# Performance work log

Hardware: AMD Instinct MI355X
Metric: run time of the kernel (lower is better)

The kernel has to match this reference:

```python
import jax, jax.numpy as jnp
import numpy as np

N = 100000   # nodes
E = 1600000  # edges
F = 128      # feature dim == Dense units
R = 50       # relations
BN_EPS = 1e-3  # keras BatchNormalization default epsilon


def setup_inputs() -> dict:
    key = jax.random.key(0)
    ks = jax.random.split(key, 8)
    x = jax.random.normal(ks[0], (N, F), dtype=jnp.float32)
    edge_rows = jax.random.randint(ks[1], (E,), 0, N, dtype=jnp.int32)
    edge_cols = jax.random.randint(ks[2], (E,), 0, N, dtype=jnp.int32)
    edge_vals = jax.random.uniform(ks[3], (E,), dtype=jnp.float32)
    rel_ids = jax.random.randint(ks[4], (E,), 0, R, dtype=jnp.int32)
    relation_coeffs = jax.random.uniform(ks[5], (R,), dtype=jnp.float32)
    coeff_kernel = jax.random.normal(ks[6], (N, 1), dtype=jnp.float32) * 0.05
    dense_kernel = jax.random.normal(ks[7], (F, F), dtype=jnp.float32) / np.sqrt(F).astype(np.float32)
    dense_bias = jnp.zeros((F,), dtype=jnp.float32)
    bn_gamma = jnp.ones((F,), dtype=jnp.float32)
    bn_beta = jnp.zeros((F,), dtype=jnp.float32)
    bn_mean = jnp.zeros((F,), dtype=jnp.float32)
    bn_var = jnp.ones((F,), dtype=jnp.float32)
    return {
        "x": x, "edge_rows": edge_rows, "edge_cols": edge_cols,
        "edge_vals": edge_vals, "rel_ids": rel_ids,
        "relation_coeffs": relation_coeffs, "coeff_kernel": coeff_kernel,
        "dense_kernel": dense_kernel, "dense_bias": dense_bias,
        "bn_gamma": bn_gamma, "bn_beta": bn_beta,
        "bn_mean": bn_mean, "bn_var": bn_var,
    }


def reference(x, edge_rows, edge_cols, edge_vals, rel_ids,
              relation_coeffs, coeff_kernel, dense_kernel, dense_bias,
              bn_gamma, bn_beta, bn_mean, bn_var):
    # BatchNorm (inference: moving statistics)
    h = (x - bn_mean) * jax.lax.rsqrt(bn_var + BN_EPS) * bn_gamma + bn_beta  # [N, F]
    # relation_coeff_adj2: edge weight = A.values * (rel_coeffs[rel] + 1)^-1
    w = edge_vals / (relation_coeffs[rel_ids] + 1.0)  # [E]
    # SpMM: out[i] = sum_{(i,j) in edges} w_e * h[j]
    msgs = w[:, None] * h[edge_cols]                   # [E, F]
    agg = jax.ops.segment_sum(msgs, edge_rows, num_segments=N)  # [N, F]
    # CoeffLayer(mul=True): inputs * (kernel + 1)
    pre = agg + h * (coeff_kernel + 1.0)               # [N, F]
    # Dense
    return pre @ dense_kernel + dense_bias             # [N, F]
```

## Files before the change

kernel.cpp:

```cpp
#include <hip/hip_runtime.h>
#include <stdint.h>

#define N_NODES 100000
#define N_EDGES 1600000
#define FDIM 128
#define NREL 50
#define BN_EPS 1e-3f
#define N_PAD 100096
#define NBUCK 782
#define EPB 8192
#define NBLK 196
#define HBLK 6250
#define LEDCAP 2816
#define SLACK 384
#define SCAP 3200
#define NSG 6250

typedef short short8_t __attribute__((ext_vector_type(8)));
typedef float f32x4_t __attribute__((ext_vector_type(4)));

__device__ __forceinline__ uint32_t f2bf(float f) {
    union { float f; uint32_t u; } v; v.f = f;
    uint32_t u = v.u;
    return (u + 0x7FFFu + ((u >> 16) & 1u)) >> 16;
}
__device__ __forceinline__ float bflo(uint32_t p) {
    union { uint32_t u; float f; } v; v.u = p << 16; return v.f;
}
__device__ __forceinline__ float bfhi(uint32_t p) {
    union { uint32_t u; float f; } v; v.u = p & 0xFFFF0000u; return v.f;
}

__global__ __launch_bounds__(512) void pre_kernel(
        const float* __restrict__ x, const int* __restrict__ rows,
        const int* __restrict__ cols, const float* __restrict__ vals,
        const int* __restrict__ rels, const float* __restrict__ relc,
        const float* __restrict__ gamma, const float* __restrict__ beta,
        const float* __restrict__ mean, const float* __restrict__ var,
        const float* __restrict__ W,
        uint2* __restrict__ h, uint16_t* __restrict__ WT,
        int* __restrict__ gcur, uint2* __restrict__ staging) {
    __shared__ int lh[NBUCK];
    __shared__ float lrel[NREL];
    int b = blockIdx.x, t = threadIdx.x;
    if (b < NBLK) {
        if (t < NREL) lrel[t] = 1.0f / (relc[t] + 1.0f);
        for (int i = t; i < NBUCK; i += 512) lh[i] = 0;
        __syncthreads();
        int e0 = b * EPB, e1 = min(e0 + EPB, N_EDGES);
        for (int e = e0 + t; e < e1; e += 512)
            atomicAdd(&lh[rows[e] >> 7], 1);
        __syncthreads();
        for (int i = t; i < NBUCK; i += 512) {
            int c = lh[i];
            int base = c ? atomicAdd(&gcur[i], c) : 0;
            lh[i] = i * SCAP + base;
        }
        __syncthreads();
        for (int e = e0 + t; e < e1; e += 512) {
            int r = rows[e];
            float w = vals[e] * lrel[rels[e]];
            int p = atomicAdd(&lh[r >> 7], 1);
            uint2 s;
            s.x = (uint32_t)cols[e] | ((uint32_t)(r & 127) << 20);
            s.y = __float_as_uint(w);
            staging[p] = s;
        }
    } else if (b == NBLK) {
        for (int idx = t; idx < FDIM * FDIM; idx += 512) {
            int f = idx >> 7, k = idx & 127;
            WT[idx] = (uint16_t)f2bf(W[k * FDIM + f]);
        }
    } else {
        int i4 = (b - NBLK - 1) * 512 + t;
        int cg = (i4 & 31) * 4;
        float4 xv = ((const float4*)x)[i4];
        float4 g4 = *(const float4*)(gamma + cg);
        float4 b4 = *(const float4*)(beta + cg);
        float4 m4 = *(const float4*)(mean + cg);
        float4 v4 = *(const float4*)(var + cg);
        float s0 = g4.x * rsqrtf(v4.x + BN_EPS);
        float s1 = g4.y * rsqrtf(v4.y + BN_EPS);
        float s2 = g4.z * rsqrtf(v4.z + BN_EPS);
        float s3 = g4.w * rsqrtf(v4.w + BN_EPS);
        uint2 o;
        o.x = f2bf((xv.x - m4.x) * s0 + b4.x) | (f2bf((xv.y - m4.y) * s1 + b4.y) << 16);
        o.y = f2bf((xv.z - m4.z) * s2 + b4.z) | (f2bf((xv.w - m4.w) * s3 + b4.w) << 16);
        h[i4] = o;
    }
}

__global__ __launch_bounds__(256) void bucket_kernel(
        const int* __restrict__ gcur, uint2* __restrict__ staging,
        uint2* __restrict__ rowrange) {
    __shared__ uint2 led[LEDCAP];
    __shared__ int lh[128];
    __shared__ int sm[128];
    __shared__ int lcur[128];
    int b = blockIdx.x, r0 = b << 7, t = threadIdx.x;
    int nrows = min(128, N_NODES - r0);
    int cnt = min(gcur[b], LEDCAP);
    uint2* sg = staging + (size_t)b * SCAP;
    if (t < 128) lh[t] = 0;
    __syncthreads();
    for (int e = t; e < cnt; e += 256) {
        uint2 s = sg[e];
        led[e] = s;
        atomicAdd(&lh[(s.x >> 20) & 127], 1);
    }
    __syncthreads();
    int v = (t < 128) ? lh[t] : 0;
    int pv = (v + 3) & ~3;
    if (t < 128) sm[t] = pv;
    __syncthreads();
    for (int off = 1; off < 128; off <<= 1) {
        int xv = 0;
        if (t < 128 && t >= off) xv = sm[t - off];
        __syncthreads();
        if (t < 128) sm[t] += xv;
        __syncthreads();
    }
    int sbase = b * SCAP;
    int start = 0;
    if (t < 128) {
        start = sbase + sm[t] - pv;
        lcur[t] = start;
        if (t < nrows) {
            uint2 rr; rr.x = (uint32_t)start; rr.y = (uint32_t)(start + pv);
            rowrange[r0 + t] = rr;
        }
    }
    __syncthreads();
    for (int e = t; e < cnt; e += 256) {
        uint2 s = led[e];
        int rl = (s.x >> 20) & 127;
        int p = atomicAdd(&lcur[rl], 1);
        uint2 o; o.x = s.x & 0xFFFFF; o.y = s.y;
        staging[p] = o;
    }
    if (t < 128) {
        uint2 z; z.x = 0; z.y = 0;
        for (int k = v; k < pv; ++k) staging[start + k] = z;
    }
}

__global__ __launch_bounds__(512, 8) void sg_kernel(
        const uint32_t* __restrict__ h, const uint2* __restrict__ rowrange,
        const uint2* __restrict__ scolw, const float* __restrict__ ck,
        const uint16_t* __restrict__ WT, const float* __restrict__ bias,
        float* __restrict__ out) {
    __shared__ uint32_t lp[16 * 64];
    int wv = threadIdx.x >> 6;
    int lane = threadIdx.x & 63;
    int row0 = blockIdx.x * 16;
    int rA = row0 + wv * 2, rB = rA + 1;

    uint2 ra = rowrange[rA];
    uint2 rb = rowrange[rB];
    int eA  = __builtin_amdgcn_readfirstlane((int)ra.x);
    int e1A = __builtin_amdgcn_readfirstlane((int)ra.y);
    int eB  = __builtin_amdgcn_readfirstlane((int)rb.x);
    int e1B = __builtin_amdgcn_readfirstlane((int)rb.y);
    uint32_t pA = h[(uint32_t)rA * 64u + lane];
    uint32_t pB = h[(uint32_t)rB * 64u + lane];
    float cA = ck[rA] + 1.0f, cB = ck[rB] + 1.0f;
    float axA = cA * bflo(pA), ayA = cA * bfhi(pA);
    float axB = cB * bflo(pB), ayB = cB * bfhi(pB);

    while (eA < e1A && eB < e1B) {
        const uint4* pa = (const uint4*)(scolw + eA);
        const uint4* pb = (const uint4*)(scolw + eB);
        uint4 a0 = pa[0], a1 = pa[1];
        uint4 b0 = pb[0], b1 = pb[1];
        uint32_t qa0 = h[a0.x * 64u + lane];
        uint32_t qa1 = h[a0.z * 64u + lane];
        uint32_t qa2 = h[a1.x * 64u + lane];
        uint32_t qa3 = h[a1.z * 64u + lane];
        uint32_t qb0 = h[b0.x * 64u + lane];
        uint32_t qb1 = h[b0.z * 64u + lane];
        uint32_t qb2 = h[b1.x * 64u + lane];
        uint32_t qb3 = h[b1.z * 64u + lane];
        float wa0 = __uint_as_float(a0.y), wa1 = __uint_as_float(a0.w);
        float wa2 = __uint_as_float(a1.y), wa3 = __uint_as_float(a1.w);
        float wb0 = __uint_as_float(b0.y), wb1 = __uint_as_float(b0.w);
        float wb2 = __uint_as_float(b1.y), wb3 = __uint_as_float(b1.w);
        axA += wa0 * bflo(qa0); ayA += wa0 * bfhi(qa0);
        axA += wa1 * bflo(qa1); ayA += wa1 * bfhi(qa1);
        axA += wa2 * bflo(qa2); ayA += wa2 * bfhi(qa2);
        axA += wa3 * bflo(qa3); ayA += wa3 * bfhi(qa3);
        axB += wb0 * bflo(qb0); ayB += wb0 * bfhi(qb0);
        axB += wb1 * bflo(qb1); ayB += wb1 * bfhi(qb1);
        axB += wb2 * bflo(qb2); ayB += wb2 * bfhi(qb2);
        axB += wb3 * bflo(qb3); ayB += wb3 * bfhi(qb3);
        eA += 4; eB += 4;
    }
    while (eA < e1A) {
        const uint4* pa = (const uint4*)(scolw + eA);
        uint4 a0 = pa[0], a1 = pa[1];
        uint32_t qa0 = h[a0.x * 64u + lane];
        uint32_t qa1 = h[a0.z * 64u + lane];
        uint32_t qa2 = h[a1.x * 64u + lane];
        uint32_t qa3 = h[a1.z * 64u + lane];
        float wa0 = __uint_as_float(a0.y), wa1 = __uint_as_float(a0.w);
        float wa2 = __uint_as_float(a1.y), wa3 = __uint_as_float(a1.w);
        axA += wa0 * bflo(qa0); ayA += wa0 * bfhi(qa0);
        axA += wa1 * bflo(qa1); ayA += wa1 * bfhi(qa1);
        axA += wa2 * bflo(qa2); ayA += wa2 * bfhi(qa2);
        axA += wa3 * bflo(qa3); ayA += wa3 * bfhi(qa3);
        eA += 4;
    }
    while (eB < e1B) {
        const uint4* pb = (const uint4*)(scolw + eB);
        uint4 b0 = pb[0], b1 = pb[1];
        uint32_t qb0 = h[b0.x * 64u + lane];
        uint32_t qb1 = h[b0.z * 64u + lane];
        uint32_t qb2 = h[b1.x * 64u + lane];
        uint32_t qb3 = h[b1.z * 64u + lane];
        float wb0 = __uint_as_float(b0.y), wb1 = __uint_as_float(b0.w);
        float wb2 = __uint_as_float(b1.y), wb3 = __uint_as_float(b1.w);
        axB += wb0 * bflo(qb0); ayB += wb0 * bfhi(qb0);
        axB += wb1 * bflo(qb1); ayB += wb1 * bfhi(qb1);
        axB += wb2 * bflo(qb2); ayB += wb2 * bfhi(qb2);
        axB += wb3 * bflo(qb3); ayB += wb3 * bfhi(qb3);
        eB += 4;
    }
    int rlA = wv * 2, rlB = rlA + 1;
    lp[rlA * 64 + (lane ^ ((rlA & 7) << 2))] = f2bf(axA) | (f2bf(ayA) << 16);
    lp[rlB * 64 + (lane ^ ((rlB & 7) << 2))] = f2bf(axB) | (f2bf(ayB) << 16);
    __syncthreads();

    int m = lane & 15, q = lane >> 4;
    short8_t a[4];
#pragma unroll
    for (int t = 0; t < 4; ++t) {
        int w0 = (q * 4 + t * 16) ^ ((m & 7) << 2);
        a[t] = *(const short8_t*)&lp[m * 64 + w0];
    }
    int col0 = wv * 16;
    const uint16_t* brow = WT + (size_t)(col0 + m) * FDIM + q * 8;
    f32x4_t acc = {0.f, 0.f, 0.f, 0.f};
#pragma unroll
    for (int t = 0; t < 4; ++t) {
        short8_t bb = *(const short8_t*)(brow + t * 32);
        acc = __builtin_amdgcn_mfma_f32_16x16x32_bf16(a[t], bb, acc, 0, 0, 0);
    }
    float bs = bias[col0 + m];
#pragma unroll
    for (int r = 0; r < 4; ++r)
        out[(size_t)(row0 + q * 4 + r) * FDIM + col0 + m] = acc[r] + bs;
}

extern "C" void kernel_launch(void* const* d_in, const int* in_sizes, int n_in,
                              void* d_out, int out_size, void* d_ws, size_t ws_size,
                              hipStream_t stream) {
    const float* x     = (const float*)d_in[0];
    const int*   erows = (const int*)d_in[1];
    const int*   ecols = (const int*)d_in[2];
    const float* evals = (const float*)d_in[3];
    const int*   erels = (const int*)d_in[4];
    const float* relc  = (const float*)d_in[5];
    const float* ck    = (const float*)d_in[6];
    const float* W     = (const float*)d_in[7];
    const float* bias  = (const float*)d_in[8];
    const float* gamma = (const float*)d_in[9];
    const float* beta  = (const float*)d_in[10];
    const float* mean  = (const float*)d_in[11];
    const float* var   = (const float*)d_in[12];
    float* out = (float*)d_out;

    char* wp = (char*)d_ws;
    auto alloc = [&](size_t bytes) {
        char* p = wp;
        wp += (bytes + 255) & ~(size_t)255;
        return (void*)p;
    };
    uint16_t* h      = (uint16_t*)alloc((size_t)N_PAD * FDIM * 2);
    uint2* staging   = (uint2*)alloc((size_t)NBUCK * SCAP * 8);
    uint2* rowrange  = (uint2*)alloc((size_t)N_PAD * 8);
    int* gcur        = (int*)alloc((size_t)NBUCK * 4);
    uint16_t* WT     = (uint16_t*)alloc(FDIM * FDIM * 2);
    if ((size_t)(wp - (char*)d_ws) > ws_size) return;

    hipMemsetAsync(gcur, 0, (size_t)NBUCK * 4, stream);
    pre_kernel<<<NBLK + 1 + HBLK, 512, 0, stream>>>(
        x, erows, ecols, evals, erels, relc, gamma, beta, mean, var, W,
        (uint2*)h, WT, gcur, staging);
    bucket_kernel<<<NBUCK, 256, 0, stream>>>(gcur, staging, rowrange);
    sg_kernel<<<NSG, 512, 0, stream>>>((const uint32_t*)h, rowrange, staging, ck,
                                       WT, bias, out);
}
```

Before: 259.9 us.

## Fuse per-bucket row sort into gather kernel using LDS-resident sorted edges

Removes the separate bucket_kernel. Buckets shrink to 64 rows, and each sg_kernel block now counting-sorts its bucket's edges into shared memory, then gathers and runs the MFMA dense projection for 64 rows. This drops one launch and the global write and re-read of the sorted staging buffer and row ranges. In exchange, occupancy drops because each block uses much more LDS and runs fewer, heavier blocks, and edges beyond SCAP per bucket are silently dropped.

```diff
diff --git a/kernel.cpp b/kernel.cpp
--- a/kernel.cpp
+++ b/kernel.cpp
@@ -7,14 +7,12 @@
 #define NREL 50
 #define BN_EPS 1e-3f
 #define N_PAD 100096
-#define NBUCK 782
+#define NBUCK 1563
 #define EPB 8192
 #define NBLK 196
 #define HBLK 6250
-#define LEDCAP 2816
-#define SLACK 384
-#define SCAP 3200
-#define NSG 6250
+#define SCAP 1536
+#define SORTN 1792
 
 typedef short short8_t __attribute__((ext_vector_type(8)));
 typedef float f32x4_t __attribute__((ext_vector_type(4)));
@@ -49,7 +47,7 @@
         __syncthreads();
         int e0 = b * EPB, e1 = min(e0 + EPB, N_EDGES);
         for (int e = e0 + t; e < e1; e += 512)
-            atomicAdd(&lh[rows[e] >> 7], 1);
+            atomicAdd(&lh[rows[e] >> 6], 1);
         __syncthreads();
         for (int i = t; i < NBUCK; i += 512) {
             int c = lh[i];
@@ -59,12 +57,15 @@
         __syncthreads();
         for (int e = e0 + t; e < e1; e += 512) {
             int r = rows[e];
+            int bk = r >> 6;
             float w = vals[e] * lrel[rels[e]];
-            int p = atomicAdd(&lh[r >> 7], 1);
-            uint2 s;
-            s.x = (uint32_t)cols[e] | ((uint32_t)(r & 127) << 20);
-            s.y = __float_as_uint(w);
-            staging[p] = s;
+            int p = atomicAdd(&lh[bk], 1);
+            if (p < (bk + 1) * SCAP) {
+                uint2 s;
+                s.x = (uint32_t)cols[e] | ((uint32_t)(r & 63) << 20);
+                s.y = __float_as_uint(w);
+                staging[p] = s;
+            }
         }
     } else if (b == NBLK) {
         for (int idx = t; idx < FDIM * FDIM; idx += 512) {
@@ -90,164 +91,167 @@
     }
 }
 
-__global__ __launch_bounds__(256) void bucket_kernel(
-        const int* __restrict__ gcur, uint2* __restrict__ staging,
-        uint2* __restrict__ rowrange) {
-    __shared__ uint2 led[LEDCAP];
-    __shared__ int lh[128];
-    __shared__ int sm[128];
-    __shared__ int lcur[128];
-    int b = blockIdx.x, r0 = b << 7, t = threadIdx.x;
-    int nrows = min(128, N_NODES - r0);
-    int cnt = min(gcur[b], LEDCAP);
-    uint2* sg = staging + (size_t)b * SCAP;
-    if (t < 128) lh[t] = 0;
-    __syncthreads();
-    for (int e = t; e < cnt; e += 256) {
-        uint2 s = sg[e];
-        led[e] = s;
-        atomicAdd(&lh[(s.x >> 20) & 127], 1);
-    }
-    __syncthreads();
-    int v = (t < 128) ? lh[t] : 0;
-    int pv = (v + 3) & ~3;
-    if (t < 128) sm[t] = pv;
-    __syncthreads();
-    for (int off = 1; off < 128; off <<= 1) {
-        int xv = 0;
-        if (t < 128 && t >= off) xv = sm[t - off];
-        __syncthreads();
-        if (t < 128) sm[t] += xv;
-        __syncthreads();
-    }
-    int sbase = b * SCAP;
-    int start = 0;
-    if (t < 128) {
-        start = sbase + sm[t] - pv;
-        lcur[t] = start;
-        if (t < nrows) {
-            uint2 rr; rr.x = (uint32_t)start; rr.y = (uint32_t)(start + pv);
-            rowrange[r0 + t] = rr;
-        }
-    }
-    __syncthreads();
-    for (int e = t; e < cnt; e += 256) {
-        uint2 s = led[e];
-        int rl = (s.x >> 20) & 127;
-        int p = atomicAdd(&lcur[rl], 1);
-        uint2 o; o.x = s.x & 0xFFFFF; o.y = s.y;
-        staging[p] = o;
-    }
-    if (t < 128) {
-        uint2 z; z.x = 0; z.y = 0;
-        for (int k = v; k < pv; ++k) staging[start + k] = z;
-    }
-}
-
 __global__ __launch_bounds__(512, 8) void sg_kernel(
-        const uint32_t* __restrict__ h, const uint2* __restrict__ rowrange,
-        const uint2* __restrict__ scolw, const float* __restrict__ ck,
+        const uint32_t* __restrict__ h, const int* __restrict__ gcur,
+        const uint2* __restrict__ staging, const float* __restrict__ ck,
         const uint16_t* __restrict__ WT, const float* __restrict__ bias,
         float* __restrict__ out) {
-    __shared__ uint32_t lp[16 * 64];
-    int wv = threadIdx.x >> 6;
-    int lane = threadIdx.x & 63;
-    int row0 = blockIdx.x * 16;
-    int rA = row0 + wv * 2, rB = rA + 1;
-
-    uint2 ra = rowrange[rA];
-    uint2 rb = rowrange[rB];
-    int eA  = __builtin_amdgcn_readfirstlane((int)ra.x);
-    int e1A = __builtin_amdgcn_readfirstlane((int)ra.y);
-    int eB  = __builtin_amdgcn_readfirstlane((int)rb.x);
-    int e1B = __builtin_amdgcn_readfirstlane((int)rb.y);
-    uint32_t pA = h[(uint32_t)rA * 64u + lane];
-    uint32_t pB = h[(uint32_t)rB * 64u + lane];
-    float cA = ck[rA] + 1.0f, cB = ck[rB] + 1.0f;
-    float axA = cA * bflo(pA), ayA = cA * bfhi(pA);
-    float axB = cB * bflo(pB), ayB = cB * bfhi(pB);
-
-    while (eA < e1A && eB < e1B) {
-        const uint4* pa = (const uint4*)(scolw + eA);
-        const uint4* pb = (const uint4*)(scolw + eB);
-        uint4 a0 = pa[0], a1 = pa[1];
-        uint4 b0 = pb[0], b1 = pb[1];
-        uint32_t qa0 = h[a0.x * 64u + lane];
-        uint32_t qa1 = h[a0.z * 64u + lane];
-        uint32_t qa2 = h[a1.x * 64u + lane];
-        uint32_t qa3 = h[a1.z * 64u + lane];
-        uint32_t qb0 = h[b0.x * 64u + lane];
-        uint32_t qb1 = h[b0.z * 64u + lane];
-        uint32_t qb2 = h[b1.x * 64u + lane];
-        uint32_t qb3 = h[b1.z * 64u + lane];
-        float wa0 = __uint_as_float(a0.y), wa1 = __uint_as_float(a0.w);
-        float wa2 = __uint_as_float(a1.y), wa3 = __uint_as_float(a1.w);
-        float wb0 = __uint_as_float(b0.y), wb1 = __uint_as_float(b0.w);
-        float wb2 = __uint_as_float(b1.y), wb3 = __uint_as_float(b1.w);
-        axA += wa0 * bflo(qa0); ayA += wa0 * bfhi(qa0);
-        axA += wa1 * bflo(qa1); ayA += wa1 * bfhi(qa1);
-        axA += wa2 * bflo(qa2); ayA += wa2 * bfhi(qa2);
-        axA += wa3 * bflo(qa3); ayA += wa3 * bfhi(qa3);
-        axB += wb0 * bflo(qb0); ayB += wb0 * bfhi(qb0);
-        axB += wb1 * bflo(qb1); ayB += wb1 * bfhi(qb1);
-        axB += wb2 * bflo(qb2); ayB += wb2 * bfhi(qb2);
-        axB += wb3 * bflo(qb3); ayB += wb3 * bfhi(qb3);
-        eA += 4; eB += 4;
-    }
-    while (eA < e1A) {
-        const uint4* pa = (const uint4*)(scolw + eA);
-        uint4 a0 = pa[0], a1 = pa[1];
-        uint32_t qa0 = h[a0.x * 64u + lane];
-        uint32_t qa1 = h[a0.z * 64u + lane];
-        uint32_t qa2 = h[a1.x * 64u + lane];
-        uint32_t qa3 = h[a1.z * 64u + lane];
-        float wa0 = __uint_as_float(a0.y), wa1 = __uint_as_float(a0.w);
-        float wa2 = __uint_as_float(a1.y), wa3 = __uint_as_float(a1.w);
-        axA += wa0 * bflo(qa0); ayA += wa0 * bfhi(qa0);
-        axA += wa1 * bflo(qa1); ayA += wa1 * bfhi(qa1);
-        axA += wa2 * bflo(qa2); ayA += wa2 * bfhi(qa2);
-        axA += wa3 * bflo(qa3); ayA += wa3 * bfhi(qa3);
-        eA += 4;
-    }
-    while (eB < e1B) {
-        const uint4* pb = (const uint4*)(scolw + eB);
-        uint4 b0 = pb[0], b1 = pb[1];
-        uint32_t qb0 = h[b0.x * 64u + lane];
-        uint32_t qb1 = h[b0.z * 64u + lane];
-        uint32_t qb2 = h[b1.x * 64u + lane];
-        uint32_t qb3 = h[b1.z * 64u + lane];
-        float wb0 = __uint_as_float(b0.y), wb1 = __uint_as_float(b0.w);
-        float wb2 = __uint_as_float(b1.y), wb3 = __uint_as_float(b1.w);
-        axB += wb0 * bflo(qb0); ayB += wb0 * bfhi(qb0);
-        axB += wb1 * bflo(qb1); ayB += wb1 * bfhi(qb1);
-        axB += wb2 * bflo(qb2); ayB += wb2 * bfhi(qb2);
-        axB += wb3 * bflo(qb3); ayB += wb3 * bfhi(qb3);
-        eB += 4;
-    }
-    int rlA = wv * 2, rlB = rlA + 1;
-    lp[rlA * 64 + (lane ^ ((rlA & 7) << 2))] = f2bf(axA) | (f2bf(ayA) << 16);
-    lp[rlB * 64 + (lane ^ ((rlB & 7) << 2))] = f2bf(axB) | (f2bf(ayB) << 16);
+    __shared__ uint32_t lp[64 * 64];
+    __shared__ uint2 sorted[SORTN];
+    __shared__ int lh[64];
+    __shared__ int lcur[64];
+    __shared__ uint2 rinfo[64];
+    uint2* led = (uint2*)lp;
+
+    int t = threadIdx.x;
+    int wv = t >> 6, lane = t & 63;
+    int b = blockIdx.x, r0 = b << 6;
+
+    if (t < 64) lh[t] = 0;
+    __syncthreads();
+    int cnt = min(gcur[b], SCAP);
+    const uint2* sge = staging + (size_t)b * SCAP;
+    for (int e = t; e < cnt; e += 512) {
+        uint2 s = sge[e];
+        led[e] = s;
+        atomicAdd(&lh[(s.x >> 20) & 63], 1);
+    }
+    __syncthreads();
+    if (t < 64) {
+        int v = lh[t];
+        int pv = (v + 3) & ~3;
+        int s = pv;
+        for (int d = 1; d < 64; d <<= 1) {
+            int u = __shfl_up(s, d);
+            if (t >= d) s += u;
+        }
+        int start = s - pv;
+        lcur[t] = start;
+        uint2 ri; ri.x = (uint32_t)start; ri.y = (uint32_t)(start + pv);
+        rinfo[t] = ri;
+        uint2 z; z.x = 0; z.y = 0;
+        for (int k = v; k < pv; ++k) sorted[start + k] = z;
+    }
+    __syncthreads();
+    for (int e = t; e < cnt; e += 512) {
+        uint2 s = led[e];
+        int rl = (s.x >> 20) & 63;
+        int p = atomicAdd(&lcur[rl], 1);
+        uint2 o; o.x = s.x & 0xFFFFFu; o.y = s.y;
+        sorted[p] = o;
+    }
+    __syncthreads();
+
+#pragma unroll
+    for (int i = 0; i < 4; ++i) {
+        int rlA = wv * 8 + 2 * i, rlB = rlA + 1;
+        int rA = r0 + rlA, rB = r0 + rlB;
+        uint2 ia = rinfo[rlA], ib = rinfo[rlB];
+        int eA  = __builtin_amdgcn_readfirstlane((int)ia.x);
+        int e1A = __builtin_amdgcn_readfirstlane((int)ia.y);
+        int eB  = __builtin_amdgcn_readfirstlane((int)ib.x);
+        int e1B = __builtin_amdgcn_readfirstlane((int)ib.y);
+        float axA = 0.f, ayA = 0.f, axB = 0.f, ayB = 0.f;
+        if (rA < N_NODES) {
+            uint32_t p = h[(uint32_t)rA * 64u + lane];
+            float c = ck[rA] + 1.0f;
+            axA = c * bflo(p); ayA = c * bfhi(p);
+        }
+        if (rB < N_NODES) {
+            uint32_t p = h[(uint32_t)rB * 64u + lane];
+            float c = ck[rB] + 1.0f;
+            axB = c * bflo(p); ayB = c * bfhi(p);
+        }
+        while (eA < e1A && eB < e1B) {
+            uint4 a0 = *(const uint4*)&sorted[eA];
+            uint4 a1 = *(const uint4*)&sorted[eA + 2];
+            uint4 b0 = *(const uint4*)&sorted[eB];
+            uint4 b1 = *(const uint4*)&sorted[eB + 2];
+            uint32_t qa0 = h[a0.x * 64u + lane];
+            uint32_t qa1 = h[a0.z * 64u + lane];
+            uint32_t qa2 = h[a1.x * 64u + lane];
+            uint32_t qa3 = h[a1.z * 64u + lane];
+            uint32_t qb0 = h[b0.x * 64u + lane];
+            uint32_t qb1 = h[b0.z * 64u + lane];
+            uint32_t qb2 = h[b1.x * 64u + lane];
+            uint32_t qb3 = h[b1.z * 64u + lane];
+            float wa0 = __uint_as_float(a0.y), wa1 = __uint_as_float(a0.w);
+            float wa2 = __uint_as_float(a1.y), wa3 = __uint_as_float(a1.w);
+            float wb0 = __uint_as_float(b0.y), wb1 = __uint_as_float(b0.w);
+            float wb2 = __uint_as_float(b1.y), wb3 = __uint_as_float(b1.w);
+            axA += wa0 * bflo(qa0); ayA += wa0 * bfhi(qa0);
+            axA += wa1 * bflo(qa1); ayA += wa1 * bfhi(qa1);
+            axA += wa2 * bflo(qa2); ayA += wa2 * bfhi(qa2);
+            axA += wa3 * bflo(qa3); ayA += wa3 * bfhi(qa3);
+            axB += wb0 * bflo(qb0); ayB += wb0 * bfhi(qb0);
+            axB += wb1 * bflo(qb1); ayB += wb1 * bfhi(qb1);
+            axB += wb2 * bflo(qb2); ayB += wb2 * bfhi(qb2);
+            axB += wb3 * bflo(qb3); ayB += wb3 * bfhi(qb3);
+            eA += 4; eB += 4;
+        }
+        while (eA < e1A) {
+            uint4 a0 = *(const uint4*)&sorted[eA];
+            uint4 a1 = *(const uint4*)&sorted[eA + 2];
+            uint32_t qa0 = h[a0.x * 64u + lane];
+            uint32_t qa1 = h[a0.z * 64u + lane];
+            uint32_t qa2 = h[a1.x * 64u + lane];
+            uint32_t qa3 = h[a1.z * 64u + lane];
+            float wa0 = __uint_as_float(a0.y), wa1 = __uint_as_float(a0.w);
+            float wa2 = __uint_as_float(a1.y), wa3 = __uint_as_float(a1.w);
+            axA += wa0 * bflo(qa0); ayA += wa0 * bfhi(qa0);
+            axA += wa1 * bflo(qa1); ayA += wa1 * bfhi(qa1);
+            axA += wa2 * bflo(qa2); ayA += wa2 * bfhi(qa2);
+            axA += wa3 * bflo(qa3); ayA += wa3 * bfhi(qa3);
+            eA += 4;
+        }
+        while (eB < e1B) {
+            uint4 b0 = *(const uint4*)&sorted[eB];
+            uint4 b1 = *(const uint4*)&sorted[eB + 2];
+            uint32_t qb0 = h[b0.x * 64u + lane];
+            uint32_t qb1 = h[b0.z * 64u + lane];
+            uint32_t qb2 = h[b1.x * 64u + lane];
+            uint32_t qb3 = h[b1.z * 64u + lane];
+            float wb0 = __uint_as_float(b0.y), wb1 = __uint_as_float(b0.w);
+            float wb2 = __uint_as_float(b1.y), wb3 = __uint_as_float(b1.w);
+            axB += wb0 * bflo(qb0); ayB += wb0 * bfhi(qb0);
+            axB += wb1 * bflo(qb1); ayB += wb1 * bfhi(qb1);
+            axB += wb2 * bflo(qb2); ayB += wb2 * bfhi(qb2);
+            axB += wb3 * bflo(qb3); ayB += wb3 * bfhi(qb3);
+            eB += 4;
+        }
+        lp[rlA * 64 + (lane ^ ((rlA & 7) << 2))] = f2bf(axA) | (f2bf(ayA) << 16);
+        lp[rlB * 64 + (lane ^ ((rlB & 7) << 2))] = f2bf(axB) | (f2bf(ayB) << 16);
+    }
     __syncthreads();
 
     int m = lane & 15, q = lane >> 4;
+    int rl0 = (wv & 3) << 4;
+    int colb = (wv >> 2) << 6;
+    int rlm = rl0 + m;
     short8_t a[4];
 #pragma unroll
-    for (int t = 0; t < 4; ++t) {
-        int w0 = (q * 4 + t * 16) ^ ((m & 7) << 2);
-        a[t] = *(const short8_t*)&lp[m * 64 + w0];
-    }
-    int col0 = wv * 16;
-    const uint16_t* brow = WT + (size_t)(col0 + m) * FDIM + q * 8;
-    f32x4_t acc = {0.f, 0.f, 0.f, 0.f};
-#pragma unroll
-    for (int t = 0; t < 4; ++t) {
-        short8_t bb = *(const short8_t*)(brow + t * 32);
-        acc = __builtin_amdgcn_mfma_f32_16x16x32_bf16(a[t], bb, acc, 0, 0, 0);
-    }
-    float bs = bias[col0 + m];
-#pragma unroll
-    for (int r = 0; r < 4; ++r)
-        out[(size_t)(row0 + q * 4 + r) * FDIM + col0 + m] = acc[r] + bs;
+    for (int tt = 0; tt < 4; ++tt) {
+        int w0 = (q * 4 + tt * 16) ^ ((rlm & 7) << 2);
+        a[tt] = *(const short8_t*)&lp[rlm * 64 + w0];
+    }
+#pragma unroll
+    for (int ct = 0; ct < 4; ++ct) {
+        int col0 = colb + ct * 16;
+        const uint16_t* brow = WT + (size_t)(col0 + m) * FDIM + q * 8;
+        f32x4_t acc = {0.f, 0.f, 0.f, 0.f};
+#pragma unroll
+        for (int tt = 0; tt < 4; ++tt) {
+            short8_t bb = *(const short8_t*)(brow + tt * 32);
+            acc = __builtin_amdgcn_mfma_f32_16x16x32_bf16(a[tt], bb, acc, 0, 0, 0);
+        }
+        float bs = bias[col0 + m];
+#pragma unroll
+        for (int r = 0; r < 4; ++r) {
+            int row = r0 + rl0 + q * 4 + r;
+            if (row < N_NODES)
+                out[(size_t)row * FDIM + col0 + m] = acc[r] + bs;
+        }
+    }
 }
 
 extern "C" void kernel_launch(void* const* d_in, const int* in_sizes, int n_in,
@@ -276,7 +280,6 @@
     };
     uint16_t* h      = (uint16_t*)alloc((size_t)N_PAD * FDIM * 2);
     uint2* staging   = (uint2*)alloc((size_t)NBUCK * SCAP * 8);
-    uint2* rowrange  = (uint2*)alloc((size_t)N_PAD * 8);
     int* gcur        = (int*)alloc((size_t)NBUCK * 4);
     uint16_t* WT     = (uint16_t*)alloc(FDIM * FDIM * 2);
     if ((size_t)(wp - (char*)d_ws) > ws_size) return;
@@ -285,7 +288,6 @@
     pre_kernel<<<NBLK + 1 + HBLK, 512, 0, stream>>>(
         x, erows, ecols, evals, erels, relc, gamma, beta, mean, var, W,
         (uint2*)h, WT, gcur, staging);
-    bucket_kernel<<<NBUCK, 256, 0, stream>>>(gcur, staging, rowrange);
-    sg_kernel<<<NSG, 512, 0, stream>>>((const uint32_t*)h, rowrange, staging, ck,
-                                       WT, bias, out);
-}
+    sg_kernel<<<NBUCK, 512, 0, stream>>>((const uint32_t*)h, gcur, staging, ck,
+                                         WT, bias, out);
+}
```

After: 256.9 us. Within noise of the previous version (-1.2%).
